# Performance work log

Measured on AMD Instinct MI355X. Metric: run time of the kernel, lower is better.

The kernel has to match this reference:

```python
import jax, jax.numpy as jnp
import numpy as np

D_MODEL, D_K, D_V, N_HEADS = 1024, 64, 64, 16
B, T = 4, 2048


def _xavier(key, shape, gain):
    fan_in, fan_out = shape[0], shape[1]
    a = gain * np.sqrt(6.0 / (fan_in + fan_out))
    return jax.random.uniform(key, shape, jnp.float32, -a, a)


def setup_inputs() -> dict:
    key = jax.random.key(0)
    ks = jax.random.split(key, 6)
    H, dk, dv, d = N_HEADS, D_K, D_V, D_MODEL
    # weights stored as (in, out) so y = x @ W matches torch nn.Linear math
    return {
        "x": jax.random.normal(ks[0], (B, T, d), jnp.float32),
        "W_q": _xavier(ks[1], (d, H * dk), 0.1),
        "W_k": _xavier(ks[2], (d, H * dk), 0.1),
        "W_v": _xavier(ks[3], (d, H * dv), 0.1),
        "W_gate": _xavier(ks[4], (d, H * dk), 0.01),
        "b_gate": jnp.full((H * dk,), 3.0, jnp.float32),
        "W_o": _xavier(ks[5], (H * dv, d), 0.1),
    }


def reference(x, W_q, W_k, W_v, W_gate, b_gate, W_o):
    Bn, Tn, d = x.shape
    H, dk, dv = N_HEADS, D_K, D_V
    q = (x @ W_q).reshape(Bn, Tn, H, dk)
    k = (x @ W_k).reshape(Bn, Tn, H, dk)
    v = (x @ W_v).reshape(Bn, Tn, H, dv)
    a = jax.nn.sigmoid(x @ W_gate + b_gate).reshape(Bn, Tn, H, dk)

    # scan over time: carry S is (B, H, dk, dv)
    def step(S, qkva):
        q_t, k_t, v_t, a_t = qkva  # each (B, H, d*)
        S = a_t[..., None] * S + k_t[..., None] * v_t[..., None, :]
        o_t = jnp.einsum('bhk,bhkv->bhv', q_t, S)
        return S, o_t

    S0 = jnp.zeros((Bn, H, dk, dv), x.dtype)
    # move time axis to front for scan
    qs = jnp.moveaxis(q, 1, 0)
    ks_ = jnp.moveaxis(k, 1, 0)
    vs = jnp.moveaxis(v, 1, 0)
    as_ = jnp.moveaxis(a, 1, 0)
    _, outs = jax.lax.scan(step, S0, (qs, ks_, vs, as_))  # (T, B, H, dv)
    out = jnp.moveaxis(outs, 0, 1).reshape(Bn, Tn, H * dv)
    return out @ W_o
```

## Files before the change

### kernel.cpp

```cpp
#include <hip/hip_runtime.h>
#include <hip/hip_bf16.h>

#define DM   1024
#define NH   16
#define TSEQ 2048
#define BBATCH 4
#define MM   (BBATCH*TSEQ)

typedef unsigned short USH;
typedef __attribute__((ext_vector_type(8))) short bf16x8;
typedef __attribute__((ext_vector_type(4))) float f32x4;

__device__ __forceinline__ USH f2bf(float f) {
  __hip_bfloat16 h = __float2bfloat16(f);
  return __builtin_bit_cast(USH, h);
}
__device__ __forceinline__ float bflo(unsigned u) { return __uint_as_float(u << 16); }
__device__ __forceinline__ float bfhi(unsigned u) { return __uint_as_float(u & 0xffff0000u); }

__device__ __forceinline__ void load16_lds(const void* g, void* l) {
  __builtin_amdgcn_global_load_lds(
      (const __attribute__((address_space(1))) unsigned int*)g,
      (__attribute__((address_space(3))) unsigned int*)l, 16, 0, 0);
}

__global__ void cvt_x(const float* __restrict__ x, USH* __restrict__ xb) {
  int i = (blockIdx.x * blockDim.x + threadIdx.x) * 4;
  float4 f = *(const float4*)(x + i);
  ushort4 u;
  u.x = f2bf(f.x); u.y = f2bf(f.y); u.z = f2bf(f.z); u.w = f2bf(f.w);
  *(ushort4*)(xb + i) = u;
}

__global__ void trans_cvt(const float* __restrict__ w0, const float* __restrict__ w1,
                          const float* __restrict__ w2, const float* __restrict__ w3,
                          const float* __restrict__ w4,
                          USH* __restrict__ wcatT, USH* __restrict__ woT) {
  int z = blockIdx.z;
  const float* src = (z == 0) ? w0 : (z == 1) ? w1 : (z == 2) ? w2 : (z == 3) ? w3 : w4;
  USH* dst = (z < 4) ? (wcatT + (size_t)z * 1024 * 1024) : woT;
  __shared__ float tile[32][33];
  int x = blockIdx.x * 32 + threadIdx.x;
  int y = blockIdx.y * 32;
  for (int j = threadIdx.y; j < 32; j += 8)
    tile[j][threadIdx.x] = src[(size_t)(y + j) * 1024 + x];
  __syncthreads();
  int x2 = blockIdx.y * 32 + threadIdx.x;
  int y2 = blockIdx.x * 32;
  for (int j = threadIdx.y; j < 32; j += 8)
    dst[(size_t)(y2 + j) * 1024 + x2] = f2bf(tile[threadIdx.x][j]);
}

template <int EPI>
__global__ __launch_bounds__(256, 2) void gemm_bt(
    const USH* __restrict__ A, const USH* __restrict__ B, int K,
    USH* __restrict__ q_out, USH* __restrict__ k_out, USH* __restrict__ v_out,
    USH* __restrict__ a_out, const float* __restrict__ bias,
    float* __restrict__ c_out) {
  __shared__ __align__(16) char smem[34816];
  short* As = (short*)smem;
  short* Bs = (short*)(smem + 16384);
  const int tid = threadIdx.x;
  const int wave = tid >> 6;
  const int lane = tid & 63;
  const int bm = blockIdx.y, bn = blockIdx.x;
  const int wm = (wave >> 1) * 64;
  const int wn = (wave & 1) * 64;

  f32x4 acc[4][4];
#pragma unroll
  for (int i = 0; i < 4; i++)
#pragma unroll
    for (int j = 0; j < 4; j++) acc[i][j] = (f32x4){0.f, 0.f, 0.f, 0.f};

  const int srow = wave * 8 + (lane >> 3);
  const int scol = ((lane & 7) ^ (lane >> 3)) * 8;

  for (int k0 = 0; k0 < K; k0 += 64) {
#pragma unroll
    for (int i = 0; i < 4; ++i) {
      int row = i * 32 + srow;
      const USH* ga = A + (size_t)(bm * 128 + row) * K + k0 + scol;
      const USH* gb = B + (size_t)(bn * 128 + row) * K + k0 + scol;
      int lofs = __builtin_amdgcn_readfirstlane((i * 32 + wave * 8) * 64);
      load16_lds(ga, (void*)(As + lofs));
      load16_lds(gb, (void*)(Bs + lofs));
    }
    __syncthreads();
    const int m16 = lane & 15;
    const int sw = lane & 7;
    const int kc = lane >> 4;
#pragma unroll
    for (int ks = 0; ks < 64; ks += 32) {
      bf16x8 af[4], bf[4];
#pragma unroll
      for (int i = 0; i < 4; i++)
        af[i] = *(const bf16x8*)&As[(wm + i * 16 + m16) * 64 + ((((ks >> 3) + kc) ^ sw) << 3)];
#pragma unroll
      for (int j = 0; j < 4; j++)
        bf[j] = *(const bf16x8*)&Bs[(wn + j * 16 + m16) * 64 + ((((ks >> 3) + kc) ^ sw) << 3)];
#pragma unroll
      for (int i = 0; i < 4; i++)
#pragma unroll
        for (int j = 0; j < 4; j++)
          acc[i][j] = __builtin_amdgcn_mfma_f32_16x16x32_bf16(af[i], bf[j], acc[i][j], 0, 0, 0);
    }
    __syncthreads();
  }

  const int r0 = (lane >> 4) * 4;
  const int cc = lane & 15;
  if (EPI == 1) {
    USH* ep = (USH*)smem;
    const int which = bn >> 3;
    float bj[4];
    if (which == 3) {
#pragma unroll
      for (int j = 0; j < 4; j++) bj[j] = bias[(bn & 7) * 128 + wn + j * 16 + cc];
    }
#pragma unroll
    for (int i = 0; i < 4; i++)
#pragma unroll
      for (int j = 0; j < 4; j++)
#pragma unroll
        for (int r = 0; r < 4; r++) {
          float val = acc[i][j][r];
          USH o;
          if (which == 3) {
            float s = 1.0f / (1.0f + __expf(-(val + bj[j])));
            o = (USH)(s * 65535.0f + 0.5f);
          } else {
            o = f2bf(val);
          }
          ep[(wm + i * 16 + r0 + r) * 136 + wn + j * 16 + cc] = o;
        }
    __syncthreads();
    USH* dst = (which == 0) ? q_out : (which == 1) ? k_out : (which == 2) ? v_out : a_out;
    const int rr = tid >> 4, ccol = (tid & 15) * 8;
#pragma unroll
    for (int it = 0; it < 8; ++it) {
      int row = it * 16 + rr;
      uint4 vd = *(const uint4*)&ep[row * 136 + ccol];
      *(uint4*)(dst + (size_t)(bm * 128 + row) * 1024 + (bn & 7) * 128 + ccol) = vd;
    }
  } else {
    float* epf = (float*)smem;
#pragma unroll
    for (int h = 0; h < 2; ++h) {
      if (wm == h * 64) {
#pragma unroll
        for (int i = 0; i < 4; i++)
#pragma unroll
          for (int j = 0; j < 4; j++)
#pragma unroll
            for (int r = 0; r < 4; r++)
              epf[(i * 16 + r0 + r) * 132 + wn + j * 16 + cc] = acc[i][j][r];
      }
      __syncthreads();
      const int rr = tid >> 5, c4 = (tid & 31) * 4;
#pragma unroll
      for (int it = 0; it < 8; ++it) {
        int row = it * 8 + rr;
        float4 vd = *(const float4*)&epf[row * 132 + c4];
        *(float4*)(c_out + (size_t)(bm * 128 + h * 64 + row) * 1024 + bn * 128 + c4) = vd;
      }
      if (h == 0) __syncthreads();
    }
  }
}

__global__ __launch_bounds__(256, 3) void gla_chunk(
    USH* __restrict__ qb, const USH* __restrict__ kb, const USH* __restrict__ vb,
    const USH* __restrict__ au, USH* __restrict__ ob,
    float* __restrict__ SB, float* __restrict__ Dc) {
  const int bh = blockIdx.x >> 5, ch = blockIdx.x & 31;
  const size_t base = (size_t)(bh >> 4) * TSEQ * 1024 + (size_t)(bh & 15) * 64;
  const int row0 = ch * 64;
  const int tid = threadIdx.x, wv = tid >> 6, ln = tid & 63;

  __shared__ __align__(16) char smem[54528];
  USH* Qs  = (USH*)smem;
  USH* Ks  = (USH*)(smem + 9216);
  USH* Kht = (USH*)(smem + 18432);
  USH* Vt  = (USH*)(smem + 27648);
  float* psum = (float*)(smem + 27648);
  USH* Ps  = (USH*)(smem + 36864);
  USH* so  = (USH*)(smem + 46080);
  float* Ag = (float*)(smem + 36864);

  {
    const int c1 = tid & 63, sg = tid >> 6;
    float lp[16], p = 1.f;
#pragma unroll
    for (int r = 0; r < 16; ++r) {
      float a = (float)au[base + (size_t)(row0 + sg * 16 + r) * 1024 + c1] * (1.f / 65535.f);
      p *= a;
      lp[r] = p;
    }
    psum[sg * 64 + c1] = p;
    __syncthreads();
    float pre = 1.f;
    for (int s2 = 0; s2 < sg; ++s2) pre *= psum[s2 * 64 + c1];
#pragma unroll
    for (int r = 0; r < 16; ++r) Ag[(sg * 16 + r) * 65 + c1] = pre * lp[r];
  }
  __syncthreads();
  if (tid < 64) Dc[((size_t)bh * 32 + ch) * 64 + tid] = Ag[63 * 65 + tid];

  {
    const int rr = tid >> 4, cg = (tid & 15) * 4;
    float AC[4];
#pragma unroll
    for (int i = 0; i < 4; i++) AC[i] = Ag[63 * 65 + cg + i];
#pragma unroll
    for (int j = 0; j < 4; ++j) {
      int row = rr + j * 16;
      size_t g = base + (size_t)(row0 + row) * 1024 + cg;
      uint2 qv = *(const uint2*)(qb + g);
      uint2 kv = *(const uint2*)(kb + g);
      uint2 vv = *(const uint2*)(vb + g);
      float A0 = Ag[row * 65 + cg], A1 = Ag[row * 65 + cg + 1];
      float A2 = Ag[row * 65 + cg + 2], A3 = Ag[row * 65 + cg + 3];
      ushort4 qt;
      qt.x = f2bf(bflo(qv.x) * A0); qt.y = f2bf(bfhi(qv.x) * A1);
      qt.z = f2bf(bflo(qv.y) * A2); qt.w = f2bf(bfhi(qv.y) * A3);
      *(ushort4*)&Qs[row * 72 + cg] = qt;
      *(ushort4*)(qb + g) = qt;
      float R0 = 1.f / A0, R1 = 1.f / A1, R2 = 1.f / A2, R3 = 1.f / A3;
      float kt0 = bflo(kv.x) * R0, kt1 = bfhi(kv.x) * R1;
      float kt2 = bflo(kv.y) * R2, kt3 = bfhi(kv.y) * R3;
      ushort4 kt;
      kt.x = f2bf(kt0); kt.y = f2bf(kt1); kt.z = f2bf(kt2); kt.w = f2bf(kt3);
      *(ushort4*)&Ks[row * 72 + cg] = kt;
      Kht[(cg + 0) * 72 + row] = f2bf(kt0 * AC[0]);
      Kht[(cg + 1) * 72 + row] = f2bf(kt1 * AC[1]);
      Kht[(cg + 2) * 72 + row] = f2bf(kt2 * AC[2]);
      Kht[(cg + 3) * 72 + row] = f2bf(kt3 * AC[3]);
      Vt[(cg + 0) * 72 + row] = (USH)(vv.x & 0xffff);
      Vt[(cg + 1) * 72 + row] = (USH)(vv.x >> 16);
      Vt[(cg + 2) * 72 + row] = (USH)(vv.y & 0xffff);
      Vt[(cg + 3) * 72 + row] = (USH)(vv.y >> 16);
    }
  }
  __syncthreads();

  const int q4 = (ln >> 4) * 4, cc = ln & 15, m16 = ln & 15;

  f32x4 pc[4];
#pragma unroll
  for (int n = 0; n < 4; n++) pc[n] = (f32x4){0.f, 0.f, 0.f, 0.f};
#pragma unroll
  for (int ks = 0; ks < 64; ks += 32) {
    bf16x8 aq = *(const bf16x8*)&Qs[(wv * 16 + m16) * 72 + ks + (ln >> 4) * 8];
#pragma unroll
    for (int n = 0; n < 4; ++n) {
      bf16x8 bk = *(const bf16x8*)&Ks[(n * 16 + m16) * 72 + ks + (ln >> 4) * 8];
      pc[n] = __builtin_amdgcn_mfma_f32_16x16x32_bf16(aq, bk, pc[n], 0, 0, 0);
    }
  }
#pragma unroll
  for (int n = 0; n < 4; ++n) {
    int s = n * 16 + cc;
#pragma unroll
    for (int r = 0; r < 4; ++r) {
      int t = wv * 16 + q4 + r;
      Ps[t * 72 + s] = f2bf(s <= t ? pc[n][r] : 0.f);
    }
  }

  f32x4 sc[4];
#pragma unroll
  for (int n = 0; n < 4; n++) sc[n] = (f32x4){0.f, 0.f, 0.f, 0.f};
#pragma unroll
  for (int ks = 0; ks < 64; ks += 32) {
    bf16x8 ak = *(const bf16x8*)&Kht[(wv * 16 + m16) * 72 + ks + (ln >> 4) * 8];
#pragma unroll
    for (int n = 0; n < 4; ++n) {
      bf16x8 bv = *(const bf16x8*)&Vt[(n * 16 + m16) * 72 + ks + (ln >> 4) * 8];
      sc[n] = __builtin_amdgcn_mfma_f32_16x16x32_bf16(ak, bv, sc[n], 0, 0, 0);
    }
  }
  {
    float* sbp = SB + ((size_t)bh * 32 + ch) * 4096;
#pragma unroll
    for (int n = 0; n < 4; ++n)
#pragma unroll
      for (int r = 0; r < 4; ++r)
        sbp[(wv * 16 + q4 + r) * 64 + n * 16 + cc] = sc[n][r];
  }
  __syncthreads();

  f32x4 oc[4];
#pragma unroll
  for (int n = 0; n < 4; n++) oc[n] = (f32x4){0.f, 0.f, 0.f, 0.f};
#pragma unroll
  for (int ks = 0; ks < 64; ks += 32) {
    bf16x8 ap = *(const bf16x8*)&Ps[(wv * 16 + m16) * 72 + ks + (ln >> 4) * 8];
#pragma unroll
    for (int n = 0; n < 4; ++n) {
      bf16x8 bv = *(const bf16x8*)&Vt[(n * 16 + m16) * 72 + ks + (ln >> 4) * 8];
      oc[n] = __builtin_amdgcn_mfma_f32_16x16x32_bf16(ap, bv, oc[n], 0, 0, 0);
    }
  }
#pragma unroll
  for (int n = 0; n < 4; ++n)
#pragma unroll
    for (int r = 0; r < 4; ++r)
      so[(wv * 16 + q4 + r) * 66 + n * 16 + cc] = f2bf(oc[n][r]);
  __syncthreads();
#pragma unroll
  for (int j = 0; j < 4; ++j) {
    int row = (tid >> 4) + j * 16, cg = (tid & 15) * 4;
    unsigned a = *(const unsigned*)&so[row * 66 + cg];
    unsigned b = *(const unsigned*)&so[row * 66 + cg + 2];
    size_t g = base + (size_t)(row0 + row) * 1024 + cg;
    *(unsigned*)(ob + g) = a;
    *(unsigned*)(ob + g + 2) = b;
  }
}

__global__ __launch_bounds__(256, 2) void gla_stitch_c(float* __restrict__ SB,
                                                       const float* __restrict__ Dc) {
  const int bh = blockIdx.x >> 2, kq = blockIdx.x & 3;
  const int tid = threadIdx.x;
  const int kk = kq * 16 + (tid >> 4);
  const int v4 = (tid & 15) * 4;
  float4 s = {0.f, 0.f, 0.f, 0.f};
  const size_t sOff = ((size_t)bh * 32) * 4096 + (size_t)kk * 64 + v4;
  const size_t dOff = ((size_t)bh * 32) * 64 + kk;
  float4 l = *(float4*)(SB + sOff);
  float D = Dc[dOff];
  for (int chn = 0; chn < 32; ++chn) {
    float4 ln2 = {0.f, 0.f, 0.f, 0.f};
    float Dn = 0.f;
    if (chn + 1 < 32) {
      ln2 = *(float4*)(SB + sOff + (size_t)(chn + 1) * 4096);
      Dn = Dc[dOff + (size_t)(chn + 1) * 64];
    }
    *(float4*)(SB + sOff + (size_t)chn * 4096) = s;
    s.x = fmaf(D, s.x, l.x); s.y = fmaf(D, s.y, l.y);
    s.z = fmaf(D, s.z, l.z); s.w = fmaf(D, s.w, l.w);
    l = ln2; D = Dn;
  }
}

__global__ __launch_bounds__(256, 4) void gla_corr(
    const USH* __restrict__ qtb, const float* __restrict__ SB, USH* __restrict__ ob) {
  const int bh = blockIdx.y, chn = blockIdx.x + 1;
  const size_t base = (size_t)(bh >> 4) * TSEQ * 1024 + (size_t)(bh & 15) * 64;
  const int trow0 = chn * 64;
  const int tid = threadIdx.x;
  __shared__ float ss[64 * 64];
  __shared__ USH qs[64][72];
  const float* sp = SB + ((size_t)bh * 32 + chn) * 4096;
  for (int i = tid; i < 1024; i += 256)
    *((float4*)ss + i) = *((const float4*)sp + i);
#pragma unroll
  for (int j = 0; j < 4; ++j) {
    int i = tid + 256 * j;
    int row = i >> 4, cg = (i & 15) * 4;
    *(uint2*)&qs[row][cg] = *(const uint2*)(qtb + base + (size_t)(trow0 + row) * 1024 + cg);
  }
  __syncthreads();
  const int row = tid >> 2, vg = (tid & 3) * 16;
  float acc[16];
#pragma unroll
  for (int i = 0; i < 16; i++) acc[i] = 0.f;
  for (int k0 = 0; k0 < 64; k0 += 8) {
    uint4 qv = *(const uint4*)&qs[row][k0];
    float qf[8];
    qf[0] = bflo(qv.x); qf[1] = bfhi(qv.x);
    qf[2] = bflo(qv.y); qf[3] = bfhi(qv.y);
    qf[4] = bflo(qv.z); qf[5] = bfhi(qv.z);
    qf[6] = bflo(qv.w); qf[7] = bfhi(qv.w);
#pragma unroll
    for (int j = 0; j < 8; ++j) {
      const float* sr = &ss[(k0 + j) * 64 + vg];
      float4 s0 = *(const float4*)(sr + 0), s1 = *(const float4*)(sr + 4);
      float4 s2 = *(const float4*)(sr + 8), s3 = *(const float4*)(sr + 12);
      acc[0] = fmaf(qf[j], s0.x, acc[0]);   acc[1] = fmaf(qf[j], s0.y, acc[1]);
      acc[2] = fmaf(qf[j], s0.z, acc[2]);   acc[3] = fmaf(qf[j], s0.w, acc[3]);
      acc[4] = fmaf(qf[j], s1.x, acc[4]);   acc[5] = fmaf(qf[j], s1.y, acc[5]);
      acc[6] = fmaf(qf[j], s1.z, acc[6]);   acc[7] = fmaf(qf[j], s1.w, acc[7]);
      acc[8] = fmaf(qf[j], s2.x, acc[8]);   acc[9] = fmaf(qf[j], s2.y, acc[9]);
      acc[10] = fmaf(qf[j], s2.z, acc[10]); acc[11] = fmaf(qf[j], s2.w, acc[11]);
      acc[12] = fmaf(qf[j], s3.x, acc[12]); acc[13] = fmaf(qf[j], s3.y, acc[13]);
      acc[14] = fmaf(qf[j], s3.z, acc[14]); acc[15] = fmaf(qf[j], s3.w, acc[15]);
    }
  }
  USH* op = ob + base + (size_t)(trow0 + row) * 1024 + vg;
#pragma unroll
  for (int g = 0; g < 4; ++g) {
    ushort4 o4 = *(ushort4*)(op + g * 4);
    o4.x = f2bf(bflo((unsigned)o4.x) + acc[g * 4 + 0]);
    o4.y = f2bf(bflo((unsigned)o4.y) + acc[g * 4 + 1]);
    o4.z = f2bf(bflo((unsigned)o4.z) + acc[g * 4 + 2]);
    o4.w = f2bf(bflo((unsigned)o4.w) + acc[g * 4 + 3]);
    *(ushort4*)(op + g * 4) = o4;
  }
}

extern "C" void kernel_launch(void* const* d_in, const int* in_sizes, int n_in,
                              void* d_out, int out_size, void* d_ws, size_t ws_size,
                              hipStream_t stream) {
  const float* x  = (const float*)d_in[0];
  const float* Wq = (const float*)d_in[1];
  const float* Wk = (const float*)d_in[2];
  const float* Wv = (const float*)d_in[3];
  const float* Wg = (const float*)d_in[4];
  const float* bg = (const float*)d_in[5];
  const float* Wo = (const float*)d_in[6];
  float* out = (float*)d_out;

  char* ws = (char*)d_ws;
  size_t off = 0;
  auto alloc = [&](size_t bytes) {
    char* p = ws + off;
    off += (bytes + 255) & ~(size_t)255;
    return p;
  };
  USH* xb   = (USH*)alloc((size_t)MM * DM * 2);
  USH* WoT  = (USH*)alloc((size_t)1024 * 1024 * 2);
  USH* qb   = (USH*)alloc((size_t)MM * DM * 2);
  USH* kb   = (USH*)alloc((size_t)MM * DM * 2);
  USH* vb   = (USH*)alloc((size_t)MM * DM * 2);
  USH* au   = (USH*)alloc((size_t)MM * DM * 2);
  float* Dc = (float*)alloc((size_t)64 * 32 * 64 * 4);
  float* SB = (float*)alloc((size_t)64 * 32 * 4096 * 4);
  USH* WcatT = (USH*)SB;
  USH* ob = xb;

  cvt_x<<<(MM * DM) / 1024, 256, 0, stream>>>(x, xb);
  trans_cvt<<<dim3(32, 32, 5), dim3(32, 8), 0, stream>>>(Wq, Wk, Wv, Wg, Wo, WcatT, WoT);
  gemm_bt<1><<<dim3(32, 64), 256, 0, stream>>>(xb, WcatT, 1024, qb, kb, vb, au, bg, nullptr);
  gla_chunk<<<2048, 256, 0, stream>>>(qb, kb, vb, au, ob, SB, Dc);
  gla_stitch_c<<<256, 256, 0, stream>>>(SB, Dc);
  gla_corr<<<dim3(31, 64), 256, 0, stream>>>(qb, SB, ob);
  gemm_bt<0><<<dim3(8, 64), 256, 0, stream>>>(ob, WoT, 1024, nullptr, nullptr, nullptr,
                                              nullptr, nullptr, out);
}
```

Measured before the change: 271.8 us.

## Fuse prep kernels, fold chunk-state stitch into last block, MFMA correction

Result: slower. 633.2 us (+133.0%).

```diff
diff --git a/kernel.cpp b/kernel.cpp
--- a/kernel.cpp
+++ b/kernel.cpp
@@ -24,31 +24,40 @@
       (__attribute__((address_space(3))) unsigned int*)l, 16, 0, 0);
 }
 
-__global__ void cvt_x(const float* __restrict__ x, USH* __restrict__ xb) {
-  int i = (blockIdx.x * blockDim.x + threadIdx.x) * 4;
-  float4 f = *(const float4*)(x + i);
-  ushort4 u;
-  u.x = f2bf(f.x); u.y = f2bf(f.y); u.z = f2bf(f.z); u.w = f2bf(f.w);
-  *(ushort4*)(xb + i) = u;
-}
-
-__global__ void trans_cvt(const float* __restrict__ w0, const float* __restrict__ w1,
-                          const float* __restrict__ w2, const float* __restrict__ w3,
-                          const float* __restrict__ w4,
-                          USH* __restrict__ wcatT, USH* __restrict__ woT) {
-  int z = blockIdx.z;
+__global__ void prep(const float* __restrict__ x, const float* __restrict__ w0,
+                     const float* __restrict__ w1, const float* __restrict__ w2,
+                     const float* __restrict__ w3, const float* __restrict__ w4,
+                     USH* __restrict__ xb, USH* __restrict__ wcatT,
+                     USH* __restrict__ woT, int* __restrict__ cnt) {
+  const int z = blockIdx.z;
+  const int tid = threadIdx.x;
+  if (z == 5) {
+    int b = blockIdx.y * 32 + blockIdx.x;
+    if (b == 0 && tid < 64) cnt[tid] = 0;
+    size_t base = (size_t)b * 8192 + tid * 4;
+#pragma unroll
+    for (int it = 0; it < 8; ++it) {
+      size_t i = base + (size_t)it * 1024;
+      float4 f = *(const float4*)(x + i);
+      ushort4 u;
+      u.x = f2bf(f.x); u.y = f2bf(f.y); u.z = f2bf(f.z); u.w = f2bf(f.w);
+      *(ushort4*)(xb + i) = u;
+    }
+    return;
+  }
   const float* src = (z == 0) ? w0 : (z == 1) ? w1 : (z == 2) ? w2 : (z == 3) ? w3 : w4;
   USH* dst = (z < 4) ? (wcatT + (size_t)z * 1024 * 1024) : woT;
   __shared__ float tile[32][33];
-  int x = blockIdx.x * 32 + threadIdx.x;
-  int y = blockIdx.y * 32;
-  for (int j = threadIdx.y; j < 32; j += 8)
-    tile[j][threadIdx.x] = src[(size_t)(y + j) * 1024 + x];
-  __syncthreads();
-  int x2 = blockIdx.y * 32 + threadIdx.x;
+  const int tx = tid & 31, ty = tid >> 5;
+  int xx = blockIdx.x * 32 + tx;
+  int yy = blockIdx.y * 32;
+  for (int j = ty; j < 32; j += 8)
+    tile[j][tx] = src[(size_t)(yy + j) * 1024 + xx];
+  __syncthreads();
+  int x2 = blockIdx.y * 32 + tx;
   int y2 = blockIdx.x * 32;
-  for (int j = threadIdx.y; j < 32; j += 8)
-    dst[(size_t)(y2 + j) * 1024 + x2] = f2bf(tile[threadIdx.x][j]);
+  for (int j = ty; j < 32; j += 8)
+    dst[(size_t)(y2 + j) * 1024 + x2] = f2bf(tile[tx][j]);
 }
 
 template <int EPI>
@@ -57,7 +66,7 @@
     USH* __restrict__ q_out, USH* __restrict__ k_out, USH* __restrict__ v_out,
     USH* __restrict__ a_out, const float* __restrict__ bias,
     float* __restrict__ c_out) {
-  __shared__ __align__(16) char smem[34816];
+  __shared__ __align__(16) char smem[32768];
   short* As = (short*)smem;
   short* Bs = (short*)(smem + 16384);
   const int tid = threadIdx.x;
@@ -132,7 +141,7 @@
           } else {
             o = f2bf(val);
           }
-          ep[(wm + i * 16 + r0 + r) * 136 + wn + j * 16 + cc] = o;
+          ep[(wm + i * 16 + r0 + r) * 128 + wn + j * 16 + cc] = o;
         }
     __syncthreads();
     USH* dst = (which == 0) ? q_out : (which == 1) ? k_out : (which == 2) ? v_out : a_out;
@@ -140,7 +149,7 @@
 #pragma unroll
     for (int it = 0; it < 8; ++it) {
       int row = it * 16 + rr;
-      uint4 vd = *(const uint4*)&ep[row * 136 + ccol];
+      uint4 vd = *(const uint4*)&ep[row * 128 + ccol];
       *(uint4*)(dst + (size_t)(bm * 128 + row) * 1024 + (bn & 7) * 128 + ccol) = vd;
     }
   } else {
@@ -154,14 +163,14 @@
           for (int j = 0; j < 4; j++)
 #pragma unroll
             for (int r = 0; r < 4; r++)
-              epf[(i * 16 + r0 + r) * 132 + wn + j * 16 + cc] = acc[i][j][r];
+              epf[(i * 16 + r0 + r) * 128 + wn + j * 16 + cc] = acc[i][j][r];
       }
       __syncthreads();
       const int rr = tid >> 5, c4 = (tid & 31) * 4;
 #pragma unroll
       for (int it = 0; it < 8; ++it) {
         int row = it * 8 + rr;
-        float4 vd = *(const float4*)&epf[row * 132 + c4];
+        float4 vd = *(const float4*)&epf[row * 128 + c4];
         *(float4*)(c_out + (size_t)(bm * 128 + h * 64 + row) * 1024 + bn * 128 + c4) = vd;
       }
       if (h == 0) __syncthreads();
@@ -172,13 +181,14 @@
 __global__ __launch_bounds__(256, 3) void gla_chunk(
     USH* __restrict__ qb, const USH* __restrict__ kb, const USH* __restrict__ vb,
     const USH* __restrict__ au, USH* __restrict__ ob,
-    float* __restrict__ SB, float* __restrict__ Dc) {
+    float* __restrict__ SB, float* __restrict__ Dc, int* __restrict__ cnt) {
   const int bh = blockIdx.x >> 5, ch = blockIdx.x & 31;
   const size_t base = (size_t)(bh >> 4) * TSEQ * 1024 + (size_t)(bh & 15) * 64;
   const int row0 = ch * 64;
   const int tid = threadIdx.x, wv = tid >> 6, ln = tid & 63;
 
   __shared__ __align__(16) char smem[54528];
+  __shared__ int lastflag;
   USH* Qs  = (USH*)smem;
   USH* Ks  = (USH*)(smem + 9216);
   USH* Kht = (USH*)(smem + 18432);
@@ -273,11 +283,11 @@
   for (int n = 0; n < 4; n++) sc[n] = (f32x4){0.f, 0.f, 0.f, 0.f};
 #pragma unroll
   for (int ks = 0; ks < 64; ks += 32) {
-    bf16x8 ak = *(const bf16x8*)&Kht[(wv * 16 + m16) * 72 + ks + (ln >> 4) * 8];
+    bf16x8 av = *(const bf16x8*)&Vt[(wv * 16 + m16) * 72 + ks + (ln >> 4) * 8];
 #pragma unroll
     for (int n = 0; n < 4; ++n) {
-      bf16x8 bv = *(const bf16x8*)&Vt[(n * 16 + m16) * 72 + ks + (ln >> 4) * 8];
-      sc[n] = __builtin_amdgcn_mfma_f32_16x16x32_bf16(ak, bv, sc[n], 0, 0, 0);
+      bf16x8 bk2 = *(const bf16x8*)&Kht[(n * 16 + m16) * 72 + ks + (ln >> 4) * 8];
+      sc[n] = __builtin_amdgcn_mfma_f32_16x16x32_bf16(av, bk2, sc[n], 0, 0, 0);
     }
   }
   {
@@ -317,30 +327,50 @@
     *(unsigned*)(ob + g) = a;
     *(unsigned*)(ob + g + 2) = b;
   }
-}
-
-__global__ __launch_bounds__(256, 2) void gla_stitch_c(float* __restrict__ SB,
-                                                       const float* __restrict__ Dc) {
-  const int bh = blockIdx.x >> 2, kq = blockIdx.x & 3;
-  const int tid = threadIdx.x;
-  const int kk = kq * 16 + (tid >> 4);
-  const int v4 = (tid & 15) * 4;
-  float4 s = {0.f, 0.f, 0.f, 0.f};
-  const size_t sOff = ((size_t)bh * 32) * 4096 + (size_t)kk * 64 + v4;
-  const size_t dOff = ((size_t)bh * 32) * 64 + kk;
-  float4 l = *(float4*)(SB + sOff);
-  float D = Dc[dOff];
-  for (int chn = 0; chn < 32; ++chn) {
-    float4 ln2 = {0.f, 0.f, 0.f, 0.f};
-    float Dn = 0.f;
-    if (chn + 1 < 32) {
-      ln2 = *(float4*)(SB + sOff + (size_t)(chn + 1) * 4096);
-      Dn = Dc[dOff + (size_t)(chn + 1) * 64];
-    }
-    *(float4*)(SB + sOff + (size_t)chn * 4096) = s;
-    s.x = fmaf(D, s.x, l.x); s.y = fmaf(D, s.y, l.y);
-    s.z = fmaf(D, s.z, l.z); s.w = fmaf(D, s.w, l.w);
-    l = ln2; D = Dn;
+
+  __threadfence();
+  if (tid == 0) {
+    int old = atomicAdd(&cnt[bh], 1);
+    lastflag = (old == 31) ? 1 : 0;
+  }
+  __syncthreads();
+  if (lastflag) {
+    __threadfence();
+    const int v = tid >> 2, kq = (tid & 3) * 16;
+    float s[16];
+#pragma unroll
+    for (int i = 0; i < 16; i++) s[i] = 0.f;
+    for (int c = 0; c < 32; ++c) {
+      float* slot = SB + ((size_t)bh * 32 + c) * 4096;
+      float4 l0 = *(float4*)(slot + v * 64 + kq + 0);
+      float4 l1 = *(float4*)(slot + v * 64 + kq + 4);
+      float4 l2 = *(float4*)(slot + v * 64 + kq + 8);
+      float4 l3 = *(float4*)(slot + v * 64 + kq + 12);
+      const float* dp = Dc + ((size_t)bh * 32 + c) * 64 + kq;
+      float4 d0 = *(const float4*)(dp + 0), d1 = *(const float4*)(dp + 4);
+      float4 d2 = *(const float4*)(dp + 8), d3 = *(const float4*)(dp + 12);
+      __syncthreads();
+      USH* up = (USH*)slot;
+      uint4 o0, o1;
+      o0.x = (unsigned)f2bf(s[0]) | ((unsigned)f2bf(s[1]) << 16);
+      o0.y = (unsigned)f2bf(s[2]) | ((unsigned)f2bf(s[3]) << 16);
+      o0.z = (unsigned)f2bf(s[4]) | ((unsigned)f2bf(s[5]) << 16);
+      o0.w = (unsigned)f2bf(s[6]) | ((unsigned)f2bf(s[7]) << 16);
+      o1.x = (unsigned)f2bf(s[8]) | ((unsigned)f2bf(s[9]) << 16);
+      o1.y = (unsigned)f2bf(s[10]) | ((unsigned)f2bf(s[11]) << 16);
+      o1.z = (unsigned)f2bf(s[12]) | ((unsigned)f2bf(s[13]) << 16);
+      o1.w = (unsigned)f2bf(s[14]) | ((unsigned)f2bf(s[15]) << 16);
+      *(uint4*)(up + v * 64 + kq + 0) = o0;
+      *(uint4*)(up + v * 64 + kq + 8) = o1;
+      s[0] = fmaf(d0.x, s[0], l0.x);  s[1] = fmaf(d0.y, s[1], l0.y);
+      s[2] = fmaf(d0.z, s[2], l0.z);  s[3] = fmaf(d0.w, s[3], l0.w);
+      s[4] = fmaf(d1.x, s[4], l1.x);  s[5] = fmaf(d1.y, s[5], l1.y);
+      s[6] = fmaf(d1.z, s[6], l1.z);  s[7] = fmaf(d1.w, s[7], l1.w);
+      s[8] = fmaf(d2.x, s[8], l2.x);  s[9] = fmaf(d2.y, s[9], l2.y);
+      s[10] = fmaf(d2.z, s[10], l2.z); s[11] = fmaf(d2.w, s[11], l2.w);
+      s[12] = fmaf(d3.x, s[12], l3.x); s[13] = fmaf(d3.y, s[13], l3.y);
+      s[14] = fmaf(d3.z, s[14], l3.z); s[15] = fmaf(d3.w, s[15], l3.w);
+    }
   }
 }
 
@@ -349,53 +379,53 @@
   const int bh = blockIdx.y, chn = blockIdx.x + 1;
   const size_t base = (size_t)(bh >> 4) * TSEQ * 1024 + (size_t)(bh & 15) * 64;
   const int trow0 = chn * 64;
-  const int tid = threadIdx.x;
-  __shared__ float ss[64 * 64];
-  __shared__ USH qs[64][72];
-  const float* sp = SB + ((size_t)bh * 32 + chn) * 4096;
-  for (int i = tid; i < 1024; i += 256)
-    *((float4*)ss + i) = *((const float4*)sp + i);
+  const int tid = threadIdx.x, wv = tid >> 6, ln = tid & 63;
+  __shared__ USH qs[64 * 72];
+  __shared__ USH sbt[64 * 72];
+  __shared__ float sof[64 * 68];
+  const USH* sp = (const USH*)(SB + ((size_t)bh * 32 + chn) * 4096);
 #pragma unroll
   for (int j = 0; j < 4; ++j) {
     int i = tid + 256 * j;
     int row = i >> 4, cg = (i & 15) * 4;
-    *(uint2*)&qs[row][cg] = *(const uint2*)(qtb + base + (size_t)(trow0 + row) * 1024 + cg);
-  }
+    *(uint2*)&qs[row * 72 + cg] = *(const uint2*)(qtb + base + (size_t)(trow0 + row) * 1024 + cg);
+    *(uint2*)&sbt[row * 72 + cg] = *(const uint2*)(sp + row * 64 + cg);
+  }
+  __syncthreads();
+  const int m16 = ln & 15, q4 = (ln >> 4) * 4, cc = ln & 15;
+  f32x4 oc[4];
+#pragma unroll
+  for (int n = 0; n < 4; n++) oc[n] = (f32x4){0.f, 0.f, 0.f, 0.f};
+#pragma unroll
+  for (int ks = 0; ks < 64; ks += 32) {
+    bf16x8 aq = *(const bf16x8*)&qs[(wv * 16 + m16) * 72 + ks + (ln >> 4) * 8];
+#pragma unroll
+    for (int n = 0; n < 4; ++n) {
+      bf16x8 bv = *(const bf16x8*)&sbt[(n * 16 + m16) * 72 + ks + (ln >> 4) * 8];
+      oc[n] = __builtin_amdgcn_mfma_f32_16x16x32_bf16(aq, bv, oc[n], 0, 0, 0);
+    }
+  }
+#pragma unroll
+  for (int n = 0; n < 4; ++n)
+#pragma unroll
+    for (int r = 0; r < 4; ++r)
+      sof[(wv * 16 + q4 + r) * 68 + n * 16 + cc] = oc[n][r];
   __syncthreads();
   const int row = tid >> 2, vg = (tid & 3) * 16;
-  float acc[16];
-#pragma unroll
-  for (int i = 0; i < 16; i++) acc[i] = 0.f;
-  for (int k0 = 0; k0 < 64; k0 += 8) {
-    uint4 qv = *(const uint4*)&qs[row][k0];
-    float qf[8];
-    qf[0] = bflo(qv.x); qf[1] = bfhi(qv.x);
-    qf[2] = bflo(qv.y); qf[3] = bfhi(qv.y);
-    qf[4] = bflo(qv.z); qf[5] = bfhi(qv.z);
-    qf[6] = bflo(qv.w); qf[7] = bfhi(qv.w);
-#pragma unroll
-    for (int j = 0; j < 8; ++j) {
-      const float* sr = &ss[(k0 + j) * 64 + vg];
-      float4 s0 = *(const float4*)(sr + 0), s1 = *(const float4*)(sr + 4);
-      float4 s2 = *(const float4*)(sr + 8), s3 = *(const float4*)(sr + 12);
-      acc[0] = fmaf(qf[j], s0.x, acc[0]);   acc[1] = fmaf(qf[j], s0.y, acc[1]);
-      acc[2] = fmaf(qf[j], s0.z, acc[2]);   acc[3] = fmaf(qf[j], s0.w, acc[3]);
-      acc[4] = fmaf(qf[j], s1.x, acc[4]);   acc[5] = fmaf(qf[j], s1.y, acc[5]);
-      acc[6] = fmaf(qf[j], s1.z, acc[6]);   acc[7] = fmaf(qf[j], s1.w, acc[7]);
-      acc[8] = fmaf(qf[j], s2.x, acc[8]);   acc[9] = fmaf(qf[j], s2.y, acc[9]);
-      acc[10] = fmaf(qf[j], s2.z, acc[10]); acc[11] = fmaf(qf[j], s2.w, acc[11]);
-      acc[12] = fmaf(qf[j], s3.x, acc[12]); acc[13] = fmaf(qf[j], s3.y, acc[13]);
-      acc[14] = fmaf(qf[j], s3.z, acc[14]); acc[15] = fmaf(qf[j], s3.w, acc[15]);
-    }
-  }
+  float4 a0 = *(const float4*)&sof[row * 68 + vg + 0];
+  float4 a1 = *(const float4*)&sof[row * 68 + vg + 4];
+  float4 a2 = *(const float4*)&sof[row * 68 + vg + 8];
+  float4 a3 = *(const float4*)&sof[row * 68 + vg + 12];
   USH* op = ob + base + (size_t)(trow0 + row) * 1024 + vg;
+  float ac[16] = {a0.x, a0.y, a0.z, a0.w, a1.x, a1.y, a1.z, a1.w,
+                  a2.x, a2.y, a2.z, a2.w, a3.x, a3.y, a3.z, a3.w};
 #pragma unroll
   for (int g = 0; g < 4; ++g) {
     ushort4 o4 = *(ushort4*)(op + g * 4);
-    o4.x = f2bf(bflo((unsigned)o4.x) + acc[g * 4 + 0]);
-    o4.y = f2bf(bflo((unsigned)o4.y) + acc[g * 4 + 1]);
-    o4.z = f2bf(bflo((unsigned)o4.z) + acc[g * 4 + 2]);
-    o4.w = f2bf(bflo((unsigned)o4.w) + acc[g * 4 + 3]);
+    o4.x = f2bf(bflo((unsigned)o4.x) + ac[g * 4 + 0]);
+    o4.y = f2bf(bflo((unsigned)o4.y) + ac[g * 4 + 1]);
+    o4.z = f2bf(bflo((unsigned)o4.z) + ac[g * 4 + 2]);
+    o4.w = f2bf(bflo((unsigned)o4.w) + ac[g * 4 + 3]);
     *(ushort4*)(op + g * 4) = o4;
   }
 }
@@ -426,15 +456,14 @@
   USH* vb   = (USH*)alloc((size_t)MM * DM * 2);
   USH* au   = (USH*)alloc((size_t)MM * DM * 2);
   float* Dc = (float*)alloc((size_t)64 * 32 * 64 * 4);
+  int* cnt  = (int*)alloc(64 * sizeof(int));
   float* SB = (float*)alloc((size_t)64 * 32 * 4096 * 4);
   USH* WcatT = (USH*)SB;
   USH* ob = xb;
 
-  cvt_x<<<(MM * DM) / 1024, 256, 0, stream>>>(x, xb);
-  trans_cvt<<<dim3(32, 32, 5), dim3(32, 8), 0, stream>>>(Wq, Wk, Wv, Wg, Wo, WcatT, WoT);
+  prep<<<dim3(32, 32, 6), 256, 0, stream>>>(x, Wq, Wk, Wv, Wg, Wo, xb, WcatT, WoT, cnt);
   gemm_bt<1><<<dim3(32, 64), 256, 0, stream>>>(xb, WcatT, 1024, qb, kb, vb, au, bg, nullptr);
-  gla_chunk<<<2048, 256, 0, stream>>>(qb, kb, vb, au, ob, SB, Dc);
-  gla_stitch_c<<<256, 256, 0, stream>>>(SB, Dc);
+  gla_chunk<<<2048, 256, 0, stream>>>(qb, kb, vb, au, ob, SB, Dc, cnt);
   gla_corr<<<dim3(31, 64), 256, 0, stream>>>(qb, SB, ob);
   gemm_bt<0><<<dim3(8, 64), 256, 0, stream>>>(ob, WoT, 1024, nullptr, nullptr, nullptr,
                                               nullptr, nullptr, out);
```
